# Optimization experiments

Hardware: AMD Instinct MI355X
Metric: run time of the kernel (lower is better)

The kernel has to match this reference:

```python
import jax, jax.numpy as jnp
import numpy as np

EPS = 1e-6
TEMP = 1.0
L = 64  # shapelet_len


def _znorm(a):
    # z-normalize over last axis, population std, clamped by EPS (matches torch unbiased=False + clamp_min)
    mean = a.mean(axis=-1, keepdims=True)
    std = jnp.maximum(a.std(axis=-1, keepdims=True), EPS)
    return (a - mean) / std


def setup_inputs() -> dict:
    key = jax.random.key(0)
    k1, k2 = jax.random.split(key)
    bs, T, C, P = 32, 8192, 1, 64
    x = jax.random.normal(k1, (bs, T, C), dtype=jnp.float32)
    shapelets = jax.random.normal(k2, (P, C, L), dtype=jnp.float32)
    return {"x": x, "shapelets": shapelets}


def reference(x, shapelets):
    # x: [bs, T, C]; shapelets: [P, C, L]
    bs, T, C = x.shape
    P = shapelets.shape[0]
    x_ct = jnp.transpose(x, (0, 2, 1))  # [bs, C, T]
    Tp = T - L + 1
    # sliding windows: [bs, C, T', L]
    idx = jnp.arange(Tp)[:, None] + jnp.arange(L)[None, :]
    w = x_ct[:, :, idx]
    # z-normalize windows and shapelets over the length axis
    w = _znorm(w)
    s = _znorm(shapelets)
    # squared euclidean distance via expansion ||w||^2 - 2 w.s + ||s||^2 (sum over C and L)
    w2 = jnp.sum(w * w, axis=(1, 3))          # [bs, T']
    s2 = jnp.sum(s * s, axis=(1, 2))          # [P]
    dot = jnp.einsum('bctl,pcl->btp', w, s)   # [bs, T', P]
    dist2 = w2[:, :, None] + s2[None, None, :] - 2.0 * dot
    temp = max(TEMP, EPS)
    act = jnp.exp(-dist2 / temp)              # [bs, T', P]
    # center-pad to length T: left = L//2, right = T - (T' + left)
    left = L // 2
    right = max(0, T - (Tp + left))
    act_full = jnp.pad(act, ((0, 0), (left, right), (0, 0)))
    return act_full[:, :T, :]
```

## Files before the change

### kernel.cpp

```cpp
#include <hip/hip_runtime.h>
#include <math.h>

#define T_LEN 8192
#define EPSF  1e-6f

typedef __attribute__((ext_vector_type(8))) short short8;
typedef __attribute__((ext_vector_type(4))) float float4v;

__global__ __launch_bounds__(256, 4) void shapelet_fused(
        const float* __restrict__ x,
        const float* __restrict__ sh,
        float* __restrict__ out) {
    __shared__ float Sraw[64][65];
    __shared__ unsigned short Bhi[64][72];
    __shared__ unsigned short Blo[64][72];
    __shared__ float xs[320];
    __shared__ float lmu[256], linv[256], lw2[256];
    __shared__ __align__(16) float lsum[64];
    __shared__ __align__(16) float ls2[64];

    const int tid  = threadIdx.x;
    const int lane = tid & 63;
    const int wave = tid >> 6;
    const int n    = lane & 15;
    const int quad = lane >> 4;

    const int super = blockIdx.x & 31;
    const int b     = blockIdx.x >> 5;
    const int t0    = super << 8;

    {
        const float4* g4 = (const float4*)sh;
#pragma unroll
        for (int i = 0; i < 4; ++i) {
            int idx = tid + (i << 8);
            float4 v = g4[idx];
            int e = idx << 2;
            int row = e >> 6, col = e & 63;
            Sraw[row][col + 0] = v.x;
            Sraw[row][col + 1] = v.y;
            Sraw[row][col + 2] = v.z;
            Sraw[row][col + 3] = v.w;
        }
        if (tid < 80) {
            int g0 = t0 - 32 + (tid << 2);
            float4 v;
            if (g0 >= 0 && g0 + 3 < T_LEN) {
                v = *(const float4*)(x + (size_t)b * T_LEN + g0);
            } else {
                float* vp = (float*)&v;
#pragma unroll
                for (int e = 0; e < 4; ++e) {
                    int g = g0 + e;
                    vp[e] = ((unsigned)g < (unsigned)T_LEN) ? x[(size_t)b * T_LEN + g] : 0.f;
                }
            }
            *(float4*)&xs[tid << 2] = v;
        }
    }
    __syncthreads();

    if (tid < 64) {
        const int p = tid;
        const int c = ((p & 3) << 4) + (p >> 2);
        float s1 = 0.f;
        for (int l = 0; l < 64; ++l) s1 += Sraw[p][l];
        float mu = s1 * (1.f / 64.f);
        float sq = 0.f;
        for (int l = 0; l < 64; ++l) { float d = Sraw[p][l] - mu; sq = fmaf(d, d, sq); }
        float sd  = fmaxf(sqrtf(sq * (1.f / 64.f)), EPSF);
        float inv = 1.f / sd;
        float ssum = 0.f, ss2 = 0.f;
        for (int l2 = 0; l2 < 32; ++l2) {
            unsigned pk_h, pk_l;
            {
                float v = Sraw[p][2 * l2];
                float s = (v - mu) * inv;
                unsigned ub = __float_as_uint(s);
                float hi = __uint_as_float(ub & 0xFFFF0000u);
                float lo = s - hi;
                unsigned lb = __float_as_uint(lo) & 0xFFFF0000u;
                pk_h = ub >> 16;
                pk_l = lb >> 16;
                float eff = hi + __uint_as_float(lb);
                ssum += eff;
                ss2  = fmaf(eff, eff, ss2);
            }
            {
                float v = Sraw[p][2 * l2 + 1];
                float s = (v - mu) * inv;
                unsigned ub = __float_as_uint(s);
                float hi = __uint_as_float(ub & 0xFFFF0000u);
                float lo = s - hi;
                unsigned lb = __float_as_uint(lo) & 0xFFFF0000u;
                pk_h |= (ub & 0xFFFF0000u);
                pk_l |= lb;
                float eff = hi + __uint_as_float(lb);
                ssum += eff;
                ss2  = fmaf(eff, eff, ss2);
            }
            *(unsigned*)&Bhi[c][2 * l2] = pk_h;
            *(unsigned*)&Blo[c][2 * l2] = pk_l;
        }
        lsum[p] = ssum;
        ls2[p]  = ss2;
    } else {
        int r = tid - 64;
#pragma unroll
        for (int pass = 0; pass < 2; ++pass) {
            if (pass == 0 || r < 64 + 192) {
                float s1 = 0.f, sq = 0.f;
#pragma unroll
                for (int l = 0; l < 64; ++l) {
                    float v = xs[r + l];
                    s1 += v; sq = fmaf(v, v, sq);
                }
                float mu  = s1 * (1.f / 64.f);
                float var = fmaxf(sq * (1.f / 64.f) - mu * mu, 0.f);
                float sd  = fmaxf(sqrtf(var), EPSF);
                float inv = 1.f / sd;
                lmu[r]  = mu;
                linv[r] = inv;
                lw2[r]  = 64.f * var * inv * inv;
            }
            if (tid >= 128) break;
            r = tid - 64 + 192;
            if (pass == 1) break;
        }
    }
    __syncthreads();

    short8 Bh[4][2], Bl[4][2];
#pragma unroll
    for (int pt = 0; pt < 4; ++pt)
#pragma unroll
        for (int h = 0; h < 2; ++h) {
            Bh[pt][h] = *(const short8*)&Bhi[pt * 16 + n][h * 32 + (quad << 3)];
            Bl[pt][h] = *(const short8*)&Blo[pt * 16 + n][h * 32 + (quad << 3)];
        }
    const float4 sm4 = *(const float4*)&lsum[n << 2];
    const float4 sv4 = *(const float4*)&ls2[n << 2];

#pragma unroll
    for (int u = 0; u < 4; ++u) {
        const int abase = (u << 6) + (wave << 4) + n + (quad << 3);
        short8 Ah[2], Al[2];
#pragma unroll
        for (int h = 0; h < 2; ++h) {
#pragma unroll
            for (int j = 0; j < 8; ++j) {
                float v = xs[abase + h * 32 + j];
                unsigned ub = __float_as_uint(v);
                unsigned hb = ub & 0xFFFF0000u;
                float lo = v - __uint_as_float(hb);
                Ah[h][j] = (short)(ub >> 16);
                Al[h][j] = (short)(__float_as_uint(lo) >> 16);
            }
        }

        float4v acc[4];
#pragma unroll
        for (int pt = 0; pt < 4; ++pt) {
            float4v a = {0.f, 0.f, 0.f, 0.f};
#pragma unroll
            for (int h = 0; h < 2; ++h) {
                a = __builtin_amdgcn_mfma_f32_16x16x32_bf16(Ah[h], Bh[pt][h], a, 0, 0, 0);
                a = __builtin_amdgcn_mfma_f32_16x16x32_bf16(Ah[h], Bl[pt][h], a, 0, 0, 0);
                a = __builtin_amdgcn_mfma_f32_16x16x32_bf16(Al[h], Bh[pt][h], a, 0, 0, 0);
            }
            acc[pt] = a;
        }

#pragma unroll
        for (int r = 0; r < 4; ++r) {
            int tl = (u << 6) + (wave << 4) + (quad << 2) + r;
            int tg = t0 + tl;
            bool valid = (tg >= 32) && (tg <= 8160);
            float mu  = lmu[tl];
            float inv = linv[tl];
            float w2  = lw2[tl];
            float d0 = (acc[0][r] - mu * sm4.x) * inv;
            float d1 = (acc[1][r] - mu * sm4.y) * inv;
            float d2 = (acc[2][r] - mu * sm4.z) * inv;
            float d3 = (acc[3][r] - mu * sm4.w) * inv;
            float4 o;
            o.x = valid ? __expf(-(w2 + sv4.x - 2.f * d0)) : 0.f;
            o.y = valid ? __expf(-(w2 + sv4.y - 2.f * d1)) : 0.f;
            o.z = valid ? __expf(-(w2 + sv4.z - 2.f * d2)) : 0.f;
            o.w = valid ? __expf(-(w2 + sv4.w - 2.f * d3)) : 0.f;
            *(float4*)(out + (((size_t)(b * T_LEN + tg)) << 6) + (n << 2)) = o;
        }
    }
}

extern "C" void kernel_launch(void* const* d_in, const int* in_sizes, int n_in,
                              void* d_out, int out_size, void* d_ws, size_t ws_size,
                              hipStream_t stream) {
    const float* x  = (const float*)d_in[0];
    const float* sh = (const float*)d_in[1];
    float* out = (float*)d_out;

    shapelet_fused<<<32 * 32, 256, 0, stream>>>(x, sh, out);
}
```

Measured before the change: 82.19 us.

## Parallelize prologue stats, pre-split x into bf16 planes, fold epilogue into exp2

Shapelet normalization is now spread across all four waves with shuffle reductions instead of one wave, and the raw shapelet staging array in shared memory is removed. Window statistics are computed by every thread from float4 partial sums, and x is converted once into hi/lo bf16 planes that the MFMA loop assembles with funnel shifts instead of re-splitting per element. The epilogue folds the log2(e) scaling and mean correction into precomputed per-row constants so each output needs one fma and a hardware exp2, and boundary masking only runs on edge blocks. The aim is to shorten the serial prologue and trim ALU work per output, at the cost of more code complexity and slightly different rounding.

Result: slower. 85.51 us (+4.0%).

```diff
diff --git a/kernel.cpp b/kernel.cpp
--- a/kernel.cpp
+++ b/kernel.cpp
@@ -3,21 +3,29 @@
 
 #define T_LEN 8192
 #define EPSF  1e-6f
+#define LOG2E 1.44269504088896340736f
 
 typedef __attribute__((ext_vector_type(8))) short short8;
 typedef __attribute__((ext_vector_type(4))) float float4v;
+
+union FragU { unsigned u[4]; short8 s; };
+
+static __device__ __forceinline__ unsigned funnel(unsigned hi, unsigned lo, unsigned s) {
+    return (unsigned)(((((unsigned long long)hi) << 32) | lo) >> s);
+}
 
 __global__ __launch_bounds__(256, 4) void shapelet_fused(
         const float* __restrict__ x,
         const float* __restrict__ sh,
         float* __restrict__ out) {
-    __shared__ float Sraw[64][65];
     __shared__ unsigned short Bhi[64][72];
     __shared__ unsigned short Blo[64][72];
     __shared__ float xs[320];
-    __shared__ float lmu[256], linv[256], lw2[256];
+    __shared__ float4 lstat[256];
     __shared__ __align__(16) float lsum[64];
     __shared__ __align__(16) float ls2[64];
+    __shared__ __align__(8) unsigned short xh16[320];
+    __shared__ __align__(8) unsigned short xl16[320];
 
     const int tid  = threadIdx.x;
     const int lane = tid & 63;
@@ -28,105 +36,142 @@
     const int super = blockIdx.x & 31;
     const int b     = blockIdx.x >> 5;
     const int t0    = super << 8;
-
+    const bool edge = (super == 0) || (super == 31);
+
+    if (tid < 80) {
+        int g0 = t0 - 32 + (tid << 2);
+        float4 v;
+        if (!edge || (g0 >= 0 && g0 + 3 < T_LEN)) {
+            v = *(const float4*)(x + (size_t)b * T_LEN + g0);
+        } else {
+            float* vp = (float*)&v;
+#pragma unroll
+            for (int e = 0; e < 4; ++e) {
+                int g = g0 + e;
+                vp[e] = ((unsigned)g < (unsigned)T_LEN) ? x[(size_t)b * T_LEN + g] : 0.f;
+            }
+        }
+        *(float4*)&xs[tid << 2] = v;
+    }
+    const int p  = (wave << 4) + (lane >> 2);
+    const int c4 = lane & 3;
+    float v[16];
     {
-        const float4* g4 = (const float4*)sh;
+        const float4* shv = (const float4*)sh;
 #pragma unroll
         for (int i = 0; i < 4; ++i) {
-            int idx = tid + (i << 8);
-            float4 v = g4[idx];
-            int e = idx << 2;
-            int row = e >> 6, col = e & 63;
-            Sraw[row][col + 0] = v.x;
-            Sraw[row][col + 1] = v.y;
-            Sraw[row][col + 2] = v.z;
-            Sraw[row][col + 3] = v.w;
-        }
-        if (tid < 80) {
-            int g0 = t0 - 32 + (tid << 2);
-            float4 v;
-            if (g0 >= 0 && g0 + 3 < T_LEN) {
-                v = *(const float4*)(x + (size_t)b * T_LEN + g0);
-            } else {
-                float* vp = (float*)&v;
-#pragma unroll
-                for (int e = 0; e < 4; ++e) {
-                    int g = g0 + e;
-                    vp[e] = ((unsigned)g < (unsigned)T_LEN) ? x[(size_t)b * T_LEN + g] : 0.f;
-                }
-            }
-            *(float4*)&xs[tid << 2] = v;
+            float4 f = shv[p * 16 + c4 * 4 + i];
+            v[i * 4 + 0] = f.x; v[i * 4 + 1] = f.y;
+            v[i * 4 + 2] = f.z; v[i * 4 + 3] = f.w;
         }
     }
     __syncthreads();
 
-    if (tid < 64) {
-        const int p = tid;
-        const int c = ((p & 3) << 4) + (p >> 2);
+    {
         float s1 = 0.f;
-        for (int l = 0; l < 64; ++l) s1 += Sraw[p][l];
+#pragma unroll
+        for (int j = 0; j < 16; ++j) s1 += v[j];
+        s1 += __shfl_xor(s1, 1);
+        s1 += __shfl_xor(s1, 2);
         float mu = s1 * (1.f / 64.f);
         float sq = 0.f;
-        for (int l = 0; l < 64; ++l) { float d = Sraw[p][l] - mu; sq = fmaf(d, d, sq); }
+#pragma unroll
+        for (int j = 0; j < 16; ++j) { float d = v[j] - mu; sq = fmaf(d, d, sq); }
+        sq += __shfl_xor(sq, 1);
+        sq += __shfl_xor(sq, 2);
         float sd  = fmaxf(sqrtf(sq * (1.f / 64.f)), EPSF);
         float inv = 1.f / sd;
+        const int c_row = ((p & 3) << 4) + (p >> 2);
         float ssum = 0.f, ss2 = 0.f;
-        for (int l2 = 0; l2 < 32; ++l2) {
-            unsigned pk_h, pk_l;
-            {
-                float v = Sraw[p][2 * l2];
-                float s = (v - mu) * inv;
-                unsigned ub = __float_as_uint(s);
+#pragma unroll
+        for (int jj = 0; jj < 4; ++jj) {
+            unsigned wh[2], wl[2];
+#pragma unroll
+            for (int k = 0; k < 2; ++k) {
+                unsigned ph = 0, pl = 0;
+#pragma unroll
+                for (int e = 0; e < 2; ++e) {
+                    float s = (v[jj * 4 + k * 2 + e] - mu) * inv;
+                    unsigned ub = __float_as_uint(s);
+                    float hi = __uint_as_float(ub & 0xFFFF0000u);
+                    float lo = s - hi;
+                    unsigned lb = __float_as_uint(lo) & 0xFFFF0000u;
+                    ph |= (e ? (ub & 0xFFFF0000u) : (ub >> 16));
+                    pl |= (e ? lb : (lb >> 16));
+                    float eff = hi + __uint_as_float(lb);
+                    ssum += eff;
+                    ss2  = fmaf(eff, eff, ss2);
+                }
+                wh[k] = ph; wl[k] = pl;
+            }
+            *(uint2*)&Bhi[c_row][c4 * 16 + jj * 4] = make_uint2(wh[0], wh[1]);
+            *(uint2*)&Blo[c_row][c4 * 16 + jj * 4] = make_uint2(wl[0], wl[1]);
+        }
+        ssum += __shfl_xor(ssum, 1);
+        ssum += __shfl_xor(ssum, 2);
+        ss2  += __shfl_xor(ss2, 1);
+        ss2  += __shfl_xor(ss2, 2);
+        if (c4 == 0) { lsum[p] = ssum; ls2[p] = ss2 * LOG2E; }
+    }
+
+    {
+        const int r = tid;
+        const int a = r >> 2, o = r & 3;
+        float fullS = 0.f, fullQ = 0.f;
+        float4 F0 = *(const float4*)&xs[a << 2];
+        fullS += F0.x + F0.y + F0.z + F0.w;
+        fullQ = fmaf(F0.x, F0.x, fmaf(F0.y, F0.y, fmaf(F0.z, F0.z, fmaf(F0.w, F0.w, fullQ))));
+#pragma unroll 4
+        for (int k = 1; k < 16; ++k) {
+            float4 f = *(const float4*)&xs[(a + k) << 2];
+            fullS += f.x + f.y + f.z + f.w;
+            fullQ = fmaf(f.x, f.x, fmaf(f.y, f.y, fmaf(f.z, f.z, fmaf(f.w, f.w, fullQ))));
+        }
+        float4 F16 = *(const float4*)&xs[(a + 16) << 2];
+        float t16S = F16.x + F16.y + F16.z + F16.w;
+        float t16Q = fmaf(F16.x, F16.x, fmaf(F16.y, F16.y, fmaf(F16.z, F16.z, F16.w * F16.w)));
+        fullS += t16S;
+        fullQ += t16Q;
+        float h0S = (o > 0 ? F0.x : 0.f) + (o > 1 ? F0.y : 0.f) + (o > 2 ? F0.z : 0.f);
+        float h0Q = (o > 0 ? F0.x * F0.x : 0.f) + (o > 1 ? F0.y * F0.y : 0.f) + (o > 2 ? F0.z * F0.z : 0.f);
+        float p16S = (o > 0 ? F16.x : 0.f) + (o > 1 ? F16.y : 0.f) + (o > 2 ? F16.z : 0.f);
+        float p16Q = (o > 0 ? F16.x * F16.x : 0.f) + (o > 1 ? F16.y * F16.y : 0.f) + (o > 2 ? F16.z * F16.z : 0.f);
+        float s1 = fullS - h0S - (t16S - p16S);
+        float sq = fullQ - h0Q - (t16Q - p16Q);
+        float mu  = s1 * (1.f / 64.f);
+        float var = fmaxf(sq * (1.f / 64.f) - mu * mu, 0.f);
+        float sd  = fmaxf(sqrtf(var), EPSF);
+        float inv = 1.f / sd;
+        float ap  = 2.f * inv * LOG2E;
+        float4 st;
+        st.x = ap;
+        st.y = ap * mu;
+        st.z = 64.f * var * inv * inv * LOG2E;
+        st.w = 0.f;
+        lstat[r] = st;
+    }
+
+    if (tid < 80) {
+        float4 f = *(const float4*)&xs[tid << 2];
+        const float* fp = (const float*)&f;
+        unsigned wh[2], wl[2];
+#pragma unroll
+        for (int k = 0; k < 2; ++k) {
+            unsigned ph = 0, pl = 0;
+#pragma unroll
+            for (int e = 0; e < 2; ++e) {
+                float vv = fp[k * 2 + e];
+                unsigned ub = __float_as_uint(vv);
                 float hi = __uint_as_float(ub & 0xFFFF0000u);
-                float lo = s - hi;
-                unsigned lb = __float_as_uint(lo) & 0xFFFF0000u;
-                pk_h = ub >> 16;
-                pk_l = lb >> 16;
-                float eff = hi + __uint_as_float(lb);
-                ssum += eff;
-                ss2  = fmaf(eff, eff, ss2);
-            }
-            {
-                float v = Sraw[p][2 * l2 + 1];
-                float s = (v - mu) * inv;
-                unsigned ub = __float_as_uint(s);
-                float hi = __uint_as_float(ub & 0xFFFF0000u);
-                float lo = s - hi;
-                unsigned lb = __float_as_uint(lo) & 0xFFFF0000u;
-                pk_h |= (ub & 0xFFFF0000u);
-                pk_l |= lb;
-                float eff = hi + __uint_as_float(lb);
-                ssum += eff;
-                ss2  = fmaf(eff, eff, ss2);
-            }
-            *(unsigned*)&Bhi[c][2 * l2] = pk_h;
-            *(unsigned*)&Blo[c][2 * l2] = pk_l;
-        }
-        lsum[p] = ssum;
-        ls2[p]  = ss2;
-    } else {
-        int r = tid - 64;
-#pragma unroll
-        for (int pass = 0; pass < 2; ++pass) {
-            if (pass == 0 || r < 64 + 192) {
-                float s1 = 0.f, sq = 0.f;
-#pragma unroll
-                for (int l = 0; l < 64; ++l) {
-                    float v = xs[r + l];
-                    s1 += v; sq = fmaf(v, v, sq);
-                }
-                float mu  = s1 * (1.f / 64.f);
-                float var = fmaxf(sq * (1.f / 64.f) - mu * mu, 0.f);
-                float sd  = fmaxf(sqrtf(var), EPSF);
-                float inv = 1.f / sd;
-                lmu[r]  = mu;
-                linv[r] = inv;
-                lw2[r]  = 64.f * var * inv * inv;
-            }
-            if (tid >= 128) break;
-            r = tid - 64 + 192;
-            if (pass == 1) break;
-        }
+                float lo = vv - hi;
+                unsigned lb = __float_as_uint(lo);
+                ph |= (e ? (ub & 0xFFFF0000u) : (ub >> 16));
+                pl |= (e ? (lb & 0xFFFF0000u) : (lb >> 16));
+            }
+            wh[k] = ph; wl[k] = pl;
+        }
+        *(uint2*)&xh16[tid << 2] = make_uint2(wh[0], wh[1]);
+        *(uint2*)&xl16[tid << 2] = make_uint2(wl[0], wl[1]);
     }
     __syncthreads();
 
@@ -140,22 +185,27 @@
         }
     const float4 sm4 = *(const float4*)&lsum[n << 2];
     const float4 sv4 = *(const float4*)&ls2[n << 2];
+    const unsigned* H = (const unsigned*)xh16;
+    const unsigned* L = (const unsigned*)xl16;
+    const unsigned shft = (n & 1) << 4;
 
 #pragma unroll
     for (int u = 0; u < 4; ++u) {
-        const int abase = (u << 6) + (wave << 4) + n + (quad << 3);
+        const int ab0 = (u << 6) + (wave << 4) + n + (quad << 3);
         short8 Ah[2], Al[2];
 #pragma unroll
         for (int h = 0; h < 2; ++h) {
-#pragma unroll
-            for (int j = 0; j < 8; ++j) {
-                float v = xs[abase + h * 32 + j];
-                unsigned ub = __float_as_uint(v);
-                unsigned hb = ub & 0xFFFF0000u;
-                float lo = v - __uint_as_float(hb);
-                Ah[h][j] = (short)(ub >> 16);
-                Al[h][j] = (short)(__float_as_uint(lo) >> 16);
-            }
+            const int i0 = (ab0 + (h << 5)) >> 1;
+            unsigned dh[5], dl[5];
+#pragma unroll
+            for (int k = 0; k < 5; ++k) { dh[k] = H[i0 + k]; dl[k] = L[i0 + k]; }
+            FragU fh, fl;
+#pragma unroll
+            for (int j = 0; j < 4; ++j) {
+                fh.u[j] = funnel(dh[j + 1], dh[j], shft);
+                fl.u[j] = funnel(dl[j + 1], dl[j], shft);
+            }
+            Ah[h] = fh.s; Al[h] = fl.s;
         }
 
         float4v acc[4];
@@ -175,19 +225,22 @@
         for (int r = 0; r < 4; ++r) {
             int tl = (u << 6) + (wave << 4) + (quad << 2) + r;
             int tg = t0 + tl;
-            bool valid = (tg >= 32) && (tg <= 8160);
-            float mu  = lmu[tl];
-            float inv = linv[tl];
-            float w2  = lw2[tl];
-            float d0 = (acc[0][r] - mu * sm4.x) * inv;
-            float d1 = (acc[1][r] - mu * sm4.y) * inv;
-            float d2 = (acc[2][r] - mu * sm4.z) * inv;
-            float d3 = (acc[3][r] - mu * sm4.w) * inv;
+            float4 st = lstat[tl];
             float4 o;
-            o.x = valid ? __expf(-(w2 + sv4.x - 2.f * d0)) : 0.f;
-            o.y = valid ? __expf(-(w2 + sv4.y - 2.f * d1)) : 0.f;
-            o.z = valid ? __expf(-(w2 + sv4.z - 2.f * d2)) : 0.f;
-            o.w = valid ? __expf(-(w2 + sv4.w - 2.f * d3)) : 0.f;
+            {
+                float u0 = fmaf(st.y, sm4.x, st.z + sv4.x);
+                float u1 = fmaf(st.y, sm4.y, st.z + sv4.y);
+                float u2 = fmaf(st.y, sm4.z, st.z + sv4.z);
+                float u3 = fmaf(st.y, sm4.w, st.z + sv4.w);
+                o.x = __builtin_amdgcn_exp2f(fmaf(st.x, acc[0][r], -u0));
+                o.y = __builtin_amdgcn_exp2f(fmaf(st.x, acc[1][r], -u1));
+                o.z = __builtin_amdgcn_exp2f(fmaf(st.x, acc[2][r], -u2));
+                o.w = __builtin_amdgcn_exp2f(fmaf(st.x, acc[3][r], -u3));
+            }
+            if (edge) {
+                bool invalid = (tg < 32) || (tg > 8160);
+                if (invalid) { o.x = 0.f; o.y = 0.f; o.z = 0.f; o.w = 0.f; }
+            }
             *(float4*)(out + (((size_t)(b * T_LEN + tg)) << 6) + (n << 2)) = o;
         }
     }
```
